# Performance work log

Hardware: AMD Instinct MI355X
Metric: run time of the kernel (lower is better)

Reference implementation:

```python
import jax, jax.numpy as jnp
import numpy as np

M = 8
EPS = 1e-5


def _bn(x, gamma, beta):
    # x: [T, N, C]; torch BatchNorm1d on [T, C, N] (training mode) normalizes
    # over batch and length dims -> axes (0, 1) here, biased variance.
    mean = jnp.mean(x, axis=(0, 1))
    var = jnp.var(x, axis=(0, 1))
    return (x - mean) * jax.lax.rsqrt(var + EPS) * gamma + beta


def setup_inputs() -> dict:
    key = jax.random.key(0)
    T, N, E = 128, 256, 128
    ks = jax.random.split(key, 16)
    s = 1.0 / np.sqrt(E)
    inp = {
        "node": jax.random.normal(ks[0], (T, N, E), dtype=jnp.float32),
        "Wq": jax.random.uniform(ks[1], (E, E), jnp.float32, -s, s),
        "bq": jax.random.uniform(ks[2], (E,), jnp.float32, -s, s),
        "Wk": jax.random.uniform(ks[3], (E, E), jnp.float32, -s, s),
        "bk": jax.random.uniform(ks[4], (E,), jnp.float32, -s, s),
        "Wv": jax.random.uniform(ks[5], (E, E), jnp.float32, -s, s),
        "bv": jax.random.uniform(ks[6], (E,), jnp.float32, -s, s),
        "Ww": jax.random.uniform(ks[7], (E, E), jnp.float32, -s, s),
        "bw": jax.random.uniform(ks[8], (E,), jnp.float32, -s, s),
        "Wf1": jax.random.uniform(ks[9], (4 * E, E), jnp.float32, -s, s),
        "bf1": jax.random.uniform(ks[10], (4 * E,), jnp.float32, -s, s),
        "Wf2": jax.random.uniform(ks[11], (E, 4 * E), jnp.float32, -0.5 * s, 0.5 * s),
        "bf2": jax.random.uniform(ks[12], (E,), jnp.float32, -0.5 * s, 0.5 * s),
        "g1": jnp.ones((E,), jnp.float32),
        "be1": jnp.zeros((E,), jnp.float32),
        "g2": jnp.ones((E,), jnp.float32),
        "be2": jnp.zeros((E,), jnp.float32),
        "temp_len": T,
    }
    return inp


def reference(node, Wq, bq, Wk, bk, Wv, bv, Ww, bw, Wf1, bf1, Wf2, bf2,
              g1, be1, g2, be2, temp_len):
    T, N, E = node.shape
    D = E // M          # head dim = 16
    dk = E / M          # softmax scale denominator (embedding_size / M)

    q = (node @ Wq.T + bq).reshape(T, N, M, D)
    k = (node @ Wk.T + bk).reshape(T, N, M, D)
    v = (node @ Wv.T + bv).reshape(T, N, M, D)

    # scores[t,n,j,m] = sum_d q[t,n,m,d]*k[t,j,m,d] / sqrt(dk)
    scores = jnp.einsum('tnmd,tjmd->tnjm', q, k) / jnp.sqrt(jnp.float32(dk))
    attn = jax.nn.softmax(scores, axis=2)  # softmax over key dim (dim=2)

    # out[t,n,m,d] = sum_j attn[t,n,j,m] * v[t,j,m,d]
    out = jnp.einsum('tnjm,tjmd->tnmd', attn, v).reshape(T, N, E)

    x = out @ Ww.T + bw + node
    x = _bn(x, g1, be1)

    x1 = jax.nn.relu(x @ Wf1.T + bf1) @ Wf2.T + bf2
    x = x + x1
    x = _bn(x, g2, be2)
    return x
```

## Files before the change

### kernel.cpp

```cpp
#include <hip/hip_runtime.h>
#include <stdint.h>

typedef unsigned int  uint32;
typedef unsigned short u16;
typedef __attribute__((ext_vector_type(8))) short short8;
typedef __attribute__((ext_vector_type(4))) float f32x4;
typedef __attribute__((ext_vector_type(4))) _Float16 half4;

__device__ __forceinline__ float bits2f(uint32 u){ union{uint32 u; float f;} c; c.u=u; return c.f; }
__device__ __forceinline__ uint32 f2bits(float f){ union{uint32 u; float f;} c; c.f=f; return c.u; }
__device__ __forceinline__ u16 f2b(float f){ uint32 u=f2bits(f); return (u16)((u + 0x7FFFu + ((u>>16)&1u))>>16); }
__device__ __forceinline__ float b2f(u16 h){ return bits2f(((uint32)h)<<16); }
__device__ __forceinline__ u16 f2h(float f){ _Float16 h=(_Float16)f; union{u16 u; _Float16 h;} c; c.h=h; return c.u; }
__device__ __forceinline__ float4 ld4f(const float* p){ return *(const float4*)p; }
#define BLO(u) bits2f((u)<<16)
#define BHI(u) bits2f((u)&0xFFFF0000u)

__global__ __launch_bounds__(256)
void cvt_w(const float4* __restrict__ wq, const float4* __restrict__ wk,
           const float4* __restrict__ wv, const float4* __restrict__ ww,
           const float4* __restrict__ wf1, const float4* __restrict__ wf2,
           u16* __restrict__ wb)
{
  const int i = blockIdx.x * 256 + threadIdx.x;
  const float4* src;
  if      (i <  4096) src = wq  + i;
  else if (i <  8192) src = wk  + (i-4096);
  else if (i < 12288) src = wv  + (i-8192);
  else if (i < 16384) src = ww  + (i-12288);
  else if (i < 32768) src = wf1 + (i-16384);
  else                src = wf2 + (i-32768);
  float4 v = *src;
  uint2 o;
  o.x = (uint32)f2b(v.x) | ((uint32)f2b(v.y) << 16);
  o.y = (uint32)f2b(v.z) | ((uint32)f2b(v.w) << 16);
  *(uint2*)(wb + (size_t)i*4) = o;
}

__device__ __forceinline__ void load_ab(const float* __restrict__ gacc,
                                        const float* __restrict__ gam,
                                        const float* __restrict__ bet,
                                        float* sA, float* sB, int t)
{
  if (t < 128) {
    const float mean = gacc[t] * (1.f/32768.f);
    const float var  = gacc[128 + t] * (1.f/32768.f) - mean * mean;
    const float rstd = rsqrtf(var + 1e-5f);
    const float Ac = gam[t] * rstd;
    sA[t] = Ac;
    sB[t] = bet[t] - mean * Ac;
  }
  __syncthreads();
}

template<int OMODE, int RES, bool RELU, bool AF32, bool BNA, bool STATS, bool ISQKV, int JT>
__global__ __launch_bounds__(256)
void gemm_k(const void* __restrict__ Ain,
            const u16* __restrict__ W0, const u16* __restrict__ W1, const u16* __restrict__ W2,
            const float* __restrict__ b0, const float* __restrict__ b1, const float* __restrict__ b2,
            const void* __restrict__ res,
            const float* __restrict__ gacc_in, const float* __restrict__ gam,
            const float* __restrict__ bet, float* __restrict__ gacc_out,
            void* __restrict__ O0, void* __restrict__ O1, void* __restrict__ O2,
            int K, int Nout, float qscale)
{
  constexpr int WROWS = JT * 32;
  __shared__ u16 As[128*72];
  __shared__ u16 Ws[WROWS*72];
  __shared__ __align__(16) float sA[128], sB[128];
  __shared__ float pS[128], pQ[128];
  const int t = threadIdx.x;
  const int row0 = blockIdx.x * 128;

  const u16* W = W0; const float* bias = b0; void* out = O0;
  float oscale = 1.f;
  int omode = OMODE, col0 = 0;
  if constexpr (ISQKV) {
    if (blockIdx.y == 1) { W = W1; bias = b1; out = O1; }
    if (blockIdx.y == 2) { W = W2; bias = b2; out = O2; omode = 3; }
    if (blockIdx.y == 0) oscale = qscale;
  } else {
    col0 = blockIdx.y * WROWS;
  }

  if constexpr (BNA || RES == 3) load_ab(gacc_in, gam, bet, sA, sB, t);

  const int L = t & 63, w = t >> 6;
  const int wrow = (w >> 1) * 64, wcol = (w & 1) * (JT * 16);
  const int lm = L & 15, lg = L >> 4;

  f32x4 acc[4][JT];
#pragma unroll
  for (int i = 0; i < 4; ++i)
#pragma unroll
    for (int j = 0; j < JT; ++j) acc[i][j] = (f32x4){0.f,0.f,0.f,0.f};

  const int srow = t >> 1, skc = (t & 1) * 32;
  const u16*   Ab = (const u16*)Ain + (size_t)(row0 + srow) * K + skc;
  const float* Af = (const float*)Ain + (size_t)(row0 + srow) * K + skc;
  u16* Asp = As + srow * 72 + skc;
  constexpr int TPR = 256 / WROWS;
  const int wsrow = t / TPR, wskc = (t % TPR) * (64 / TPR);
  const u16* Wp = W + (size_t)(col0 + wsrow) * K + wskc;
  u16* Wsp = Ws + wsrow * 72 + wskc;
  constexpr int NW = (64 / TPR) / 8;

  for (int k0 = 0; k0 < K; k0 += 64) {
    short8 ga[4], gw[NW];
    if constexpr (AF32) {
#pragma unroll
      for (int i = 0; i < 4; ++i) {
        const float4 fa = ld4f(Af + k0 + i*8);
        const float4 fb = ld4f(Af + k0 + i*8 + 4);
        short8 s;
        s[0]=(short)f2b(fa.x); s[1]=(short)f2b(fa.y); s[2]=(short)f2b(fa.z); s[3]=(short)f2b(fa.w);
        s[4]=(short)f2b(fb.x); s[5]=(short)f2b(fb.y); s[6]=(short)f2b(fb.z); s[7]=(short)f2b(fb.w);
        ga[i] = s;
      }
    } else if constexpr (BNA) {
#pragma unroll
      for (int i = 0; i < 4; ++i) {
        const int c = skc + k0 + i*8;
        const short8 x8 = *(const short8*)(Ab + k0 + i*8);
        const float4 A0 = *(const float4*)&sA[c], A1 = *(const float4*)&sA[c+4];
        const float4 B0 = *(const float4*)&sB[c], B1 = *(const float4*)&sB[c+4];
        short8 s;
        s[0]=(short)f2b(b2f((u16)x8[0])*A0.x+B0.x); s[1]=(short)f2b(b2f((u16)x8[1])*A0.y+B0.y);
        s[2]=(short)f2b(b2f((u16)x8[2])*A0.z+B0.z); s[3]=(short)f2b(b2f((u16)x8[3])*A0.w+B0.w);
        s[4]=(short)f2b(b2f((u16)x8[4])*A1.x+B1.x); s[5]=(short)f2b(b2f((u16)x8[5])*A1.y+B1.y);
        s[6]=(short)f2b(b2f((u16)x8[6])*A1.z+B1.z); s[7]=(short)f2b(b2f((u16)x8[7])*A1.w+B1.w);
        ga[i] = s;
      }
    } else {
#pragma unroll
      for (int i = 0; i < 4; ++i) ga[i] = *(const short8*)(Ab + k0 + i*8);
    }
#pragma unroll
    for (int i = 0; i < NW; ++i) gw[i] = *(const short8*)(Wp + k0 + i*8);
    __syncthreads();
#pragma unroll
    for (int i = 0; i < 4; ++i) *(short8*)(Asp + i*8) = ga[i];
#pragma unroll
    for (int i = 0; i < NW; ++i) *(short8*)(Wsp + i*8) = gw[i];
    __syncthreads();
#pragma unroll
    for (int ks = 0; ks < 64; ks += 32) {
      short8 af[4], wf[JT];
#pragma unroll
      for (int i = 0; i < 4; ++i)
        af[i] = *(const short8*)(As + (wrow + i*16 + lm) * 72 + ks + lg*8);
#pragma unroll
      for (int j = 0; j < JT; ++j)
        wf[j] = *(const short8*)(Ws + (wcol + j*16 + lm) * 72 + ks + lg*8);
#pragma unroll
      for (int i = 0; i < 4; ++i)
#pragma unroll
        for (int j = 0; j < JT; ++j)
          acc[i][j] = __builtin_amdgcn_mfma_f32_16x16x32_bf16(af[i], wf[j], acc[i][j], 0, 0, 0);
    }
  }

  float bj[JT];
#pragma unroll
  for (int j = 0; j < JT; ++j) bj[j] = bias[col0 + wcol + j*16 + lm];

  float stS[JT], stQ[JT];
#pragma unroll
  for (int j = 0; j < JT; ++j) { stS[j] = 0.f; stQ[j] = 0.f; }

#pragma unroll
  for (int i = 0; i < 4; ++i) {
    const int rowb = row0 + wrow + i*16 + lg*4;
#pragma unroll
    for (int j = 0; j < JT; ++j) {
      const int col = col0 + wcol + j*16 + lm;
      float ra = 0.f, rb = 0.f;
      if constexpr (RES == 3) { ra = sA[col & 127]; rb = sB[col & 127]; }
      if (omode == 3) {
        const int tt = rowb >> 8, n0 = rowb & 255;
        const int mh = col >> 4, d = col & 15;
        uint2 o;
        o.x = (uint32)f2h(acc[i][j][0] + bj[j]) | ((uint32)f2h(acc[i][j][1] + bj[j]) << 16);
        o.y = (uint32)f2h(acc[i][j][2] + bj[j]) | ((uint32)f2h(acc[i][j][3] + bj[j]) << 16);
        *(uint2*)((u16*)out + (((size_t)tt*8 + mh)*16 + d)*256 + n0) = o;
      } else {
#pragma unroll
        for (int r = 0; r < 4; ++r) {
          const int row = rowb + r;
          float v = acc[i][j][r] + bj[j];
          if constexpr (RES == 1) v += ((const float*)res)[(size_t)row*128 + col];
          if constexpr (RES == 3) v += b2f(((const u16*)res)[(size_t)row*128 + col]) * ra + rb;
          if constexpr (RELU) v = fmaxf(v, 0.f);
          if constexpr (STATS) { stS[j] += v; stQ[j] += v*v; }
          if (omode == 2) {
            const int tt = row >> 8, n = row & 255, mh = col >> 4, d = col & 15;
            ((u16*)out)[(((size_t)tt*8 + mh)*256 + n)*16 + d] = f2h(v * oscale);
          } else {
            ((u16*)out)[(size_t)row * Nout + col] = f2b(v);
          }
        }
      }
    }
  }

  if constexpr (STATS) {
    __syncthreads();
    if (t < 128) { pS[t] = 0.f; pQ[t] = 0.f; }
    __syncthreads();
#pragma unroll
    for (int j = 0; j < JT; ++j) {
      const int col = col0 + wcol + j*16 + lm;
      atomicAdd(&pS[col], stS[j]);
      atomicAdd(&pQ[col], stQ[j]);
    }
    __syncthreads();
    if (t < 128) {
      atomicAdd(&gacc_out[t],       pS[t]);
      atomicAdd(&gacc_out[128 + t], pQ[t]);
    }
  }
}

#define QKS 24
__global__ __launch_bounds__(256)
void attn_k(const u16* __restrict__ q, const u16* __restrict__ k,
            const u16* __restrict__ v, u16* __restrict__ ab)
{
  __shared__ __align__(16) u16 Qs[256*QKS];
  __shared__ __align__(16) u16 Ks[256*QKS];
  __shared__ __align__(16) u16 Vt[16*264];
  const int tm = blockIdx.x, tt = tm >> 3, m = tm & 7;
  const int t = threadIdx.x;

  const uint4* qg = (const uint4*)(q + (size_t)tm*4096);
  const uint4* kg = (const uint4*)(k + (size_t)tm*4096);
  const uint4* vg = (const uint4*)(v + (size_t)tm*4096);
#pragma unroll
  for (int p = t; p < 512; p += 256) {
    const uint4 a = qg[p], b = kg[p], c = vg[p];
    const int row = p >> 1, h = (p & 1) * 8;
    *(uint4*)(Qs + row*QKS + h) = a;
    *(uint4*)(Ks + row*QKS + h) = b;
    *(uint4*)(Vt + (p >> 5)*264 + (p & 31)*8) = c;
  }
  __syncthreads();

  const int w = t >> 6, L = t & 63, lm = L & 15, quad = L >> 4;

  half4 vf[16];
#pragma unroll
  for (int jt = 0; jt < 16; ++jt)
    vf[jt] = *(const half4*)(Vt + lm*264 + jt*16 + quad*4);

  for (int nt = 0; nt < 4; ++nt) {
    const half4 bq = *(const half4*)(Qs + ((w*4 + nt)*16 + lm)*QKS + quad*4);
    f32x4 s[16];
#pragma unroll
    for (int jt = 0; jt < 16; ++jt) {
      const half4 af = *(const half4*)(Ks + (jt*16 + lm)*QKS + quad*4);
      s[jt] = __builtin_amdgcn_mfma_f32_16x16x16f16(af, bq, (f32x4){0.f,0.f,0.f,0.f}, 0, 0, 0);
    }
    float mx = s[0][0];
#pragma unroll
    for (int jt = 0; jt < 16; ++jt)
#pragma unroll
      for (int r = 0; r < 4; ++r) mx = fmaxf(mx, s[jt][r]);
    mx = fmaxf(mx, __shfl_xor(mx, 16));
    mx = fmaxf(mx, __shfl_xor(mx, 32));
    float ls = 0.f;
#pragma unroll
    for (int jt = 0; jt < 16; ++jt)
#pragma unroll
      for (int r = 0; r < 4; ++r) { const float p = exp2f(s[jt][r] - mx); s[jt][r] = p; ls += p; }
    ls += __shfl_xor(ls, 16);
    ls += __shfl_xor(ls, 32);

    f32x4 oacc = {0.f,0.f,0.f,0.f};
#pragma unroll
    for (int jt = 0; jt < 16; ++jt) {
      half4 pf;
      pf[0] = (_Float16)s[jt][0]; pf[1] = (_Float16)s[jt][1];
      pf[2] = (_Float16)s[jt][2]; pf[3] = (_Float16)s[jt][3];
      oacc = __builtin_amdgcn_mfma_f32_16x16x16f16(pf, vf[jt], oacc, 0, 0, 0);
    }
    const int q0 = w*64 + nt*16 + quad*4;
#pragma unroll
    for (int r = 0; r < 4; ++r) {
      const float lr = __shfl(ls, quad*4 + r);
      ab[((size_t)tt*256 + q0 + r)*128 + m*16 + lm] = f2b(oacc[r] / lr);
    }
  }
}

__global__ __launch_bounds__(256)
void bn_final(const uint32* __restrict__ x2, const float* __restrict__ gacc,
              const float* __restrict__ gam, const float* __restrict__ bet,
              float* __restrict__ out)
{
  __shared__ float sA[128], sB[128];
  const int t = threadIdx.x;
  load_ab(gacc, gam, bet, sA, sB, t);
#pragma unroll 4
  for (int kk = 0; kk < 32; ++kk) {
    const size_t idx = (size_t)blockIdx.x * 8192 + kk * 256 + t;
    const uint32 u = x2[idx];
    const int c = (int)((idx & 63) * 2);
    float2 o;
    o.x = BLO(u) * sA[c]   + sB[c];
    o.y = BHI(u) * sA[c+1] + sB[c+1];
    ((float2*)out)[idx] = o;
  }
}

extern "C" void kernel_launch(void* const* d_in, const int* in_sizes, int n_in,
                              void* d_out, int out_size, void* d_ws, size_t ws_size,
                              hipStream_t stream)
{
  (void)in_sizes; (void)n_in; (void)out_size; (void)ws_size;
  const float* node = (const float*)d_in[0];
  const float* Wq  = (const float*)d_in[1];  const float* bq  = (const float*)d_in[2];
  const float* Wk  = (const float*)d_in[3];  const float* bk  = (const float*)d_in[4];
  const float* Wv  = (const float*)d_in[5];  const float* bv  = (const float*)d_in[6];
  const float* Ww  = (const float*)d_in[7];  const float* bw  = (const float*)d_in[8];
  const float* Wf1 = (const float*)d_in[9];  const float* bf1 = (const float*)d_in[10];
  const float* Wf2 = (const float*)d_in[11]; const float* bf2 = (const float*)d_in[12];
  const float* g1  = (const float*)d_in[13]; const float* be1 = (const float*)d_in[14];
  const float* g2  = (const float*)d_in[15]; const float* be2 = (const float*)d_in[16];
  float* out = (float*)d_out;
  char* ws = (char*)d_ws;

  u16* wb  = (u16*)(ws + 0);
  u16* qb  = (u16*)(ws + 524288);
  u16* kb  = (u16*)(ws + 8912896);
  u16* vb  = (u16*)(ws + 17301504);
  u16* ab  = (u16*)(ws + 25690112);
  u16* xb  = (u16*)(ws + 34078720);
  u16* x2b = (u16*)(ws + 42467328);
  float* accbuf = (float*)(ws + 50855936);
  u16* hb  = qb;

  u16* wqb = wb;          u16* wkb = wb + 16384;  u16* wvb = wb + 32768;
  u16* wwb = wb + 49152;  u16* wf1b = wb + 65536; u16* wf2b = wb + 131072;

  dim3 blk(256);
  const float QSCALE = 0.36067376022224085f;

  hipMemsetAsync(accbuf, 0, 512 * sizeof(float), stream);
  cvt_w<<<dim3(192), blk, 0, stream>>>((const float4*)Wq, (const float4*)Wk,
      (const float4*)Wv, (const float4*)Ww, (const float4*)Wf1, (const float4*)Wf2, wb);

  gemm_k<2,0,false,true,false,false,true,4><<<dim3(256,3), blk, 0, stream>>>(
      node, wqb,wkb,wvb, bq,bk,bv, nullptr, nullptr,nullptr,nullptr,nullptr,
      qb,kb,vb, 128, 128, QSCALE);

  attn_k<<<dim3(1024), blk, 0, stream>>>(qb, kb, vb, ab);

  gemm_k<0,1,false,false,false,true,false,4><<<dim3(256,1), blk, 0, stream>>>(
      ab, wwb,wwb,wwb, bw,bw,bw, node, nullptr,nullptr,nullptr, accbuf,
      xb,xb,xb, 128, 128, 1.f);

  gemm_k<0,0,true,false,true,false,false,4><<<dim3(256,4), blk, 0, stream>>>(
      xb, wf1b,wf1b,wf1b, bf1,bf1,bf1, nullptr, accbuf,g1,be1, nullptr,
      hb,hb,hb, 128, 512, 1.f);

  gemm_k<0,3,false,false,false,true,false,2><<<dim3(256,2), blk, 0, stream>>>(
      hb, wf2b,wf2b,wf2b, bf2,bf2,bf2, xb, accbuf,g1,be1, accbuf + 256,
      x2b,x2b,x2b, 512, 128, 1.f);

  bn_final<<<dim3(256), blk, 0, stream>>>((const uint32*)x2b, accbuf + 256, g2, be2, out);
}
```

Measured before the change: 209.0 us.

## Fuse all stages into one persistent kernel with software grid barriers

Merges the weight conversion, QKV GEMM, attention, output projection, FFN GEMMs and final batch-norm into one persistent kernel of 512 blocks. Stages are separated by an atomic-counter grid barrier and work is distributed with grid-stride loops over tiles. This removes six kernel launches and the gaps between them. In exchange it depends on all 512 blocks being co-resident (launch bounds set to 2 blocks per CU), adds spin-wait barrier cost, and uses a union of shared memory that may lower occupancy.

```diff
diff --git a/kernel.cpp b/kernel.cpp
--- a/kernel.cpp
+++ b/kernel.cpp
@@ -16,25 +16,58 @@
 #define BLO(u) bits2f((u)<<16)
 #define BHI(u) bits2f((u)&0xFFFF0000u)
 
-__global__ __launch_bounds__(256)
-void cvt_w(const float4* __restrict__ wq, const float4* __restrict__ wk,
-           const float4* __restrict__ wv, const float4* __restrict__ ww,
-           const float4* __restrict__ wf1, const float4* __restrict__ wf2,
-           u16* __restrict__ wb)
-{
-  const int i = blockIdx.x * 256 + threadIdx.x;
+#define QKS 24
+#define GRID 512
+
+struct Params {
+  const float* node;
+  const float *Wq,*bq,*Wk,*bk,*Wv,*bv,*Ww,*bw,*Wf1,*bf1,*Wf2,*bf2;
+  const float *g1,*be1,*g2,*be2;
+  float* out;
+  u16 *wb, *qb, *kb, *vb, *ab, *xb, *x2b, *hb;
+  float* accbuf;
+  int *cnt, *gen;
+};
+
+union SharedU {
+  struct { u16 As[128*72]; u16 Ws[128*72]; } g;
+  struct { u16 Qs[256*QKS]; u16 Ks[256*QKS]; u16 Vt[16*264]; } a;
+};
+
+__device__ __forceinline__ void gbar(int* cnt, int* gen)
+{
+  __syncthreads();
+  if (threadIdx.x == 0) {
+    __threadfence();
+    const int g = __hip_atomic_load(gen, __ATOMIC_RELAXED, __HIP_MEMORY_SCOPE_AGENT);
+    const int a = __hip_atomic_fetch_add(cnt, 1, __ATOMIC_ACQ_REL, __HIP_MEMORY_SCOPE_AGENT);
+    if (a == GRID - 1) {
+      __hip_atomic_store(cnt, 0, __ATOMIC_RELAXED, __HIP_MEMORY_SCOPE_AGENT);
+      __hip_atomic_fetch_add(gen, 1, __ATOMIC_RELEASE, __HIP_MEMORY_SCOPE_AGENT);
+    } else {
+      while (__hip_atomic_load(gen, __ATOMIC_RELAXED, __HIP_MEMORY_SCOPE_AGENT) == g)
+        __builtin_amdgcn_s_sleep(8);
+    }
+    __threadfence();
+  }
+  __syncthreads();
+}
+
+__device__ __forceinline__ void cvt_job(const Params& p, int j, int t)
+{
+  const int i = j * 256 + t;
   const float4* src;
-  if      (i <  4096) src = wq  + i;
-  else if (i <  8192) src = wk  + (i-4096);
-  else if (i < 12288) src = wv  + (i-8192);
-  else if (i < 16384) src = ww  + (i-12288);
-  else if (i < 32768) src = wf1 + (i-16384);
-  else                src = wf2 + (i-32768);
+  if      (i <  4096) src = (const float4*)p.Wq  + i;
+  else if (i <  8192) src = (const float4*)p.Wk  + (i-4096);
+  else if (i < 12288) src = (const float4*)p.Wv  + (i-8192);
+  else if (i < 16384) src = (const float4*)p.Ww  + (i-12288);
+  else if (i < 32768) src = (const float4*)p.Wf1 + (i-16384);
+  else                src = (const float4*)p.Wf2 + (i-32768);
   float4 v = *src;
   uint2 o;
   o.x = (uint32)f2b(v.x) | ((uint32)f2b(v.y) << 16);
   o.y = (uint32)f2b(v.z) | ((uint32)f2b(v.w) << 16);
-  *(uint2*)(wb + (size_t)i*4) = o;
+  *(uint2*)(p.wb + (size_t)i*4) = o;
 }
 
 __device__ __forceinline__ void load_ab(const float* __restrict__ gacc,
@@ -53,38 +86,16 @@
   __syncthreads();
 }
 
-template<int OMODE, int RES, bool RELU, bool AF32, bool BNA, bool STATS, bool ISQKV, int JT>
-__global__ __launch_bounds__(256)
-void gemm_k(const void* __restrict__ Ain,
-            const u16* __restrict__ W0, const u16* __restrict__ W1, const u16* __restrict__ W2,
-            const float* __restrict__ b0, const float* __restrict__ b1, const float* __restrict__ b2,
-            const void* __restrict__ res,
-            const float* __restrict__ gacc_in, const float* __restrict__ gam,
-            const float* __restrict__ bet, float* __restrict__ gacc_out,
-            void* __restrict__ O0, void* __restrict__ O1, void* __restrict__ O2,
-            int K, int Nout, float qscale)
+template<int OMODE, int RES, bool RELU, bool AF32, bool BNA, bool STATS, int JT>
+__device__ __forceinline__ void gemm_tile(
+    SharedU* Up, const float* sA, const float* sB, float* pS, float* pQ,
+    const void* Ain, const u16* W, const float* bias, const void* res,
+    float* gacc_out, void* out, int row0, int col0, int K, int Nout,
+    float oscale, int t)
 {
   constexpr int WROWS = JT * 32;
-  __shared__ u16 As[128*72];
-  __shared__ u16 Ws[WROWS*72];
-  __shared__ __align__(16) float sA[128], sB[128];
-  __shared__ float pS[128], pQ[128];
-  const int t = threadIdx.x;
-  const int row0 = blockIdx.x * 128;
-
-  const u16* W = W0; const float* bias = b0; void* out = O0;
-  float oscale = 1.f;
-  int omode = OMODE, col0 = 0;
-  if constexpr (ISQKV) {
-    if (blockIdx.y == 1) { W = W1; bias = b1; out = O1; }
-    if (blockIdx.y == 2) { W = W2; bias = b2; out = O2; omode = 3; }
-    if (blockIdx.y == 0) oscale = qscale;
-  } else {
-    col0 = blockIdx.y * WROWS;
-  }
-
-  if constexpr (BNA || RES == 3) load_ab(gacc_in, gam, bet, sA, sB, t);
-
+  u16* As = Up->g.As;
+  u16* Ws = Up->g.Ws;
   const int L = t & 63, w = t >> 6;
   const int wrow = (w >> 1) * 64, wcol = (w & 1) * (JT * 16);
   const int lm = L & 15, lg = L >> 4;
@@ -176,7 +187,7 @@
       const int col = col0 + wcol + j*16 + lm;
       float ra = 0.f, rb = 0.f;
       if constexpr (RES == 3) { ra = sA[col & 127]; rb = sB[col & 127]; }
-      if (omode == 3) {
+      if constexpr (OMODE == 3) {
         const int tt = rowb >> 8, n0 = rowb & 255;
         const int mh = col >> 4, d = col & 15;
         uint2 o;
@@ -192,7 +203,7 @@
           if constexpr (RES == 3) v += b2f(((const u16*)res)[(size_t)row*128 + col]) * ra + rb;
           if constexpr (RELU) v = fmaxf(v, 0.f);
           if constexpr (STATS) { stS[j] += v; stQ[j] += v*v; }
-          if (omode == 2) {
+          if constexpr (OMODE == 2) {
             const int tt = row >> 8, n = row & 255, mh = col >> 4, d = col & 15;
             ((u16*)out)[(((size_t)tt*8 + mh)*256 + n)*16 + d] = f2h(v * oscale);
           } else {
@@ -221,20 +232,16 @@
   }
 }
 
-#define QKS 24
-__global__ __launch_bounds__(256)
-void attn_k(const u16* __restrict__ q, const u16* __restrict__ k,
-            const u16* __restrict__ v, u16* __restrict__ ab)
-{
-  __shared__ __align__(16) u16 Qs[256*QKS];
-  __shared__ __align__(16) u16 Ks[256*QKS];
-  __shared__ __align__(16) u16 Vt[16*264];
-  const int tm = blockIdx.x, tt = tm >> 3, m = tm & 7;
-  const int t = threadIdx.x;
+__device__ __forceinline__ void attn_job(SharedU* Up, const u16* q, const u16* k,
+                                         const u16* v, u16* ab, int tm, int t)
+{
+  u16* Qs = Up->a.Qs; u16* Ks = Up->a.Ks; u16* Vt = Up->a.Vt;
+  const int tt = tm >> 3, m = tm & 7;
 
   const uint4* qg = (const uint4*)(q + (size_t)tm*4096);
   const uint4* kg = (const uint4*)(k + (size_t)tm*4096);
   const uint4* vg = (const uint4*)(v + (size_t)tm*4096);
+  __syncthreads();
 #pragma unroll
   for (int p = t; p < 512; p += 256) {
     const uint4 a = qg[p], b = kg[p], c = vg[p];
@@ -292,23 +299,69 @@
   }
 }
 
-__global__ __launch_bounds__(256)
-void bn_final(const uint32* __restrict__ x2, const float* __restrict__ gacc,
-              const float* __restrict__ gam, const float* __restrict__ bet,
-              float* __restrict__ out)
-{
-  __shared__ float sA[128], sB[128];
-  const int t = threadIdx.x;
-  load_ab(gacc, gam, bet, sA, sB, t);
+__global__ __launch_bounds__(256, 2)
+void fused_k(Params p)
+{
+  __shared__ __align__(16) SharedU U;
+  __shared__ __align__(16) float sA[128], sB[128];
+  __shared__ float pS[128], pQ[128];
+  const int t = threadIdx.x, bid = blockIdx.x;
+  const float QSCALE = 0.36067376022224085f;
+
+  const u16* wqb = p.wb;          const u16* wkb = p.wb + 16384;  const u16* wvb = p.wb + 32768;
+  const u16* wwb = p.wb + 49152;  const u16* wf1b = p.wb + 65536; const u16* wf2b = p.wb + 131072;
+
+  for (int j = bid; j < 192; j += GRID) cvt_job(p, j, t);
+  gbar(p.cnt, p.gen);
+
+  for (int j = bid; j < 768; j += GRID) {
+    const int x = j & 255, y = j >> 8;
+    if (y == 0)
+      gemm_tile<2,0,false,true,false,false,4>(&U,sA,sB,pS,pQ, p.node, wqb, p.bq,
+          nullptr, nullptr, p.qb, x*128, 0, 128, 128, QSCALE, t);
+    else if (y == 1)
+      gemm_tile<2,0,false,true,false,false,4>(&U,sA,sB,pS,pQ, p.node, wkb, p.bk,
+          nullptr, nullptr, p.kb, x*128, 0, 128, 128, 1.f, t);
+    else
+      gemm_tile<3,0,false,true,false,false,4>(&U,sA,sB,pS,pQ, p.node, wvb, p.bv,
+          nullptr, nullptr, p.vb, x*128, 0, 128, 128, 1.f, t);
+  }
+  gbar(p.cnt, p.gen);
+
+  for (int j = bid; j < 1024; j += GRID) attn_job(&U, p.qb, p.kb, p.vb, p.ab, j, t);
+  gbar(p.cnt, p.gen);
+
+  for (int j = bid; j < 256; j += GRID)
+    gemm_tile<0,1,false,false,false,true,4>(&U,sA,sB,pS,pQ, p.ab, wwb, p.bw,
+        p.node, p.accbuf, p.xb, j*128, 0, 128, 128, 1.f, t);
+  gbar(p.cnt, p.gen);
+
+  load_ab(p.accbuf, p.g1, p.be1, sA, sB, t);
+  for (int j = bid; j < 1024; j += GRID) {
+    const int x = j & 255, cy = j >> 8;
+    gemm_tile<0,0,true,false,true,false,4>(&U,sA,sB,pS,pQ, p.xb, wf1b, p.bf1,
+        nullptr, nullptr, p.hb, x*128, cy*128, 128, 512, 1.f, t);
+  }
+  gbar(p.cnt, p.gen);
+
+  for (int j = bid; j < 512; j += GRID)
+    gemm_tile<0,3,false,false,false,true,2>(&U,sA,sB,pS,pQ, p.hb, wf2b, p.bf2,
+        p.xb, p.accbuf + 256, p.x2b, (j >> 1)*128, (j & 1)*64, 512, 128, 1.f, t);
+  gbar(p.cnt, p.gen);
+
+  load_ab(p.accbuf + 256, p.g2, p.be2, sA, sB, t);
+  const uint32* x2 = (const uint32*)p.x2b;
+  for (int j = bid; j < 512; j += GRID) {
 #pragma unroll 4
-  for (int kk = 0; kk < 32; ++kk) {
-    const size_t idx = (size_t)blockIdx.x * 8192 + kk * 256 + t;
-    const uint32 u = x2[idx];
-    const int c = (int)((idx & 63) * 2);
-    float2 o;
-    o.x = BLO(u) * sA[c]   + sB[c];
-    o.y = BHI(u) * sA[c+1] + sB[c+1];
-    ((float2*)out)[idx] = o;
+    for (int kk = 0; kk < 16; ++kk) {
+      const size_t idx = (size_t)j * 4096 + kk * 256 + t;
+      const uint32 u = x2[idx];
+      const int c = (int)((idx & 63) * 2);
+      float2 o;
+      o.x = BLO(u) * sA[c]   + sB[c];
+      o.y = BHI(u) * sA[c+1] + sB[c+1];
+      ((float2*)p.out)[idx] = o;
+    }
   }
 }
 
@@ -317,55 +370,33 @@
                               hipStream_t stream)
 {
   (void)in_sizes; (void)n_in; (void)out_size; (void)ws_size;
-  const float* node = (const float*)d_in[0];
-  const float* Wq  = (const float*)d_in[1];  const float* bq  = (const float*)d_in[2];
-  const float* Wk  = (const float*)d_in[3];  const float* bk  = (const float*)d_in[4];
-  const float* Wv  = (const float*)d_in[5];  const float* bv  = (const float*)d_in[6];
-  const float* Ww  = (const float*)d_in[7];  const float* bw  = (const float*)d_in[8];
-  const float* Wf1 = (const float*)d_in[9];  const float* bf1 = (const float*)d_in[10];
-  const float* Wf2 = (const float*)d_in[11]; const float* bf2 = (const float*)d_in[12];
-  const float* g1  = (const float*)d_in[13]; const float* be1 = (const float*)d_in[14];
-  const float* g2  = (const float*)d_in[15]; const float* be2 = (const float*)d_in[16];
-  float* out = (float*)d_out;
   char* ws = (char*)d_ws;
 
-  u16* wb  = (u16*)(ws + 0);
-  u16* qb  = (u16*)(ws + 524288);
-  u16* kb  = (u16*)(ws + 8912896);
-  u16* vb  = (u16*)(ws + 17301504);
-  u16* ab  = (u16*)(ws + 25690112);
-  u16* xb  = (u16*)(ws + 34078720);
-  u16* x2b = (u16*)(ws + 42467328);
-  float* accbuf = (float*)(ws + 50855936);
-  u16* hb  = qb;
-
-  u16* wqb = wb;          u16* wkb = wb + 16384;  u16* wvb = wb + 32768;
-  u16* wwb = wb + 49152;  u16* wf1b = wb + 65536; u16* wf2b = wb + 131072;
-
-  dim3 blk(256);
-  const float QSCALE = 0.36067376022224085f;
-
-  hipMemsetAsync(accbuf, 0, 512 * sizeof(float), stream);
-  cvt_w<<<dim3(192), blk, 0, stream>>>((const float4*)Wq, (const float4*)Wk,
-      (const float4*)Wv, (const float4*)Ww, (const float4*)Wf1, (const float4*)Wf2, wb);
-
-  gemm_k<2,0,false,true,false,false,true,4><<<dim3(256,3), blk, 0, stream>>>(
-      node, wqb,wkb,wvb, bq,bk,bv, nullptr, nullptr,nullptr,nullptr,nullptr,
-      qb,kb,vb, 128, 128, QSCALE);
-
-  attn_k<<<dim3(1024), blk, 0, stream>>>(qb, kb, vb, ab);
-
-  gemm_k<0,1,false,false,false,true,false,4><<<dim3(256,1), blk, 0, stream>>>(
-      ab, wwb,wwb,wwb, bw,bw,bw, node, nullptr,nullptr,nullptr, accbuf,
-      xb,xb,xb, 128, 128, 1.f);
-
-  gemm_k<0,0,true,false,true,false,false,4><<<dim3(256,4), blk, 0, stream>>>(
-      xb, wf1b,wf1b,wf1b, bf1,bf1,bf1, nullptr, accbuf,g1,be1, nullptr,
-      hb,hb,hb, 128, 512, 1.f);
-
-  gemm_k<0,3,false,false,false,true,false,2><<<dim3(256,2), blk, 0, stream>>>(
-      hb, wf2b,wf2b,wf2b, bf2,bf2,bf2, xb, accbuf,g1,be1, accbuf + 256,
-      x2b,x2b,x2b, 512, 128, 1.f);
-
-  bn_final<<<dim3(256), blk, 0, stream>>>((const uint32*)x2b, accbuf + 256, g2, be2, out);
-}
+  Params P;
+  P.node = (const float*)d_in[0];
+  P.Wq  = (const float*)d_in[1];  P.bq  = (const float*)d_in[2];
+  P.Wk  = (const float*)d_in[3];  P.bk  = (const float*)d_in[4];
+  P.Wv  = (const float*)d_in[5];  P.bv  = (const float*)d_in[6];
+  P.Ww  = (const float*)d_in[7];  P.bw  = (const float*)d_in[8];
+  P.Wf1 = (const float*)d_in[9];  P.bf1 = (const float*)d_in[10];
+  P.Wf2 = (const float*)d_in[11]; P.bf2 = (const float*)d_in[12];
+  P.g1  = (const float*)d_in[13]; P.be1 = (const float*)d_in[14];
+  P.g2  = (const float*)d_in[15]; P.be2 = (const float*)d_in[16];
+  P.out = (float*)d_out;
+
+  P.wb  = (u16*)(ws + 0);
+  P.qb  = (u16*)(ws + 524288);
+  P.kb  = (u16*)(ws + 8912896);
+  P.vb  = (u16*)(ws + 17301504);
+  P.ab  = (u16*)(ws + 25690112);
+  P.xb  = (u16*)(ws + 34078720);
+  P.x2b = (u16*)(ws + 42467328);
+  P.accbuf = (float*)(ws + 50855936);
+  P.cnt = (int*)(ws + 50855936 + 2048);
+  P.gen = (int*)(ws + 50855936 + 2052);
+  P.hb  = P.qb;
+
+  hipMemsetAsync(ws + 50855936, 0, 4096, stream);
+
+  fused_k<<<dim3(GRID), dim3(256), 0, stream>>>(P);
+}
```

Result: slower. 579.5 us (+177.3%).

## Fuse weight conversion, memset and QKV GEMM into one launch

Applied to the files above, without the earlier changes.

Removes the separate memset and weight-conversion kernel. The QKV projection now reads fp32 weights and converts them inline, while extra blocks in the same launch convert the remaining weights to bf16 and zero the stats accumulators. GEMM kernels become per-stage wrappers around a shared device tile routine with compile-time output modes, and bn_final uses twice as many blocks. This cuts launch count and serial dependencies, at the cost of each QKV block re-converting the fp32 weights.

```diff
diff --git a/kernel.cpp b/kernel.cpp
--- a/kernel.cpp
+++ b/kernel.cpp
@@ -16,26 +16,7 @@
 #define BLO(u) bits2f((u)<<16)
 #define BHI(u) bits2f((u)&0xFFFF0000u)
 
-__global__ __launch_bounds__(256)
-void cvt_w(const float4* __restrict__ wq, const float4* __restrict__ wk,
-           const float4* __restrict__ wv, const float4* __restrict__ ww,
-           const float4* __restrict__ wf1, const float4* __restrict__ wf2,
-           u16* __restrict__ wb)
-{
-  const int i = blockIdx.x * 256 + threadIdx.x;
-  const float4* src;
-  if      (i <  4096) src = wq  + i;
-  else if (i <  8192) src = wk  + (i-4096);
-  else if (i < 12288) src = wv  + (i-8192);
-  else if (i < 16384) src = ww  + (i-12288);
-  else if (i < 32768) src = wf1 + (i-16384);
-  else                src = wf2 + (i-32768);
-  float4 v = *src;
-  uint2 o;
-  o.x = (uint32)f2b(v.x) | ((uint32)f2b(v.y) << 16);
-  o.y = (uint32)f2b(v.z) | ((uint32)f2b(v.w) << 16);
-  *(uint2*)(wb + (size_t)i*4) = o;
-}
+#define QKS 24
 
 __device__ __forceinline__ void load_ab(const float* __restrict__ gacc,
                                         const float* __restrict__ gam,
@@ -53,38 +34,14 @@
   __syncthreads();
 }
 
-template<int OMODE, int RES, bool RELU, bool AF32, bool BNA, bool STATS, bool ISQKV, int JT>
-__global__ __launch_bounds__(256)
-void gemm_k(const void* __restrict__ Ain,
-            const u16* __restrict__ W0, const u16* __restrict__ W1, const u16* __restrict__ W2,
-            const float* __restrict__ b0, const float* __restrict__ b1, const float* __restrict__ b2,
-            const void* __restrict__ res,
-            const float* __restrict__ gacc_in, const float* __restrict__ gam,
-            const float* __restrict__ bet, float* __restrict__ gacc_out,
-            void* __restrict__ O0, void* __restrict__ O1, void* __restrict__ O2,
-            int K, int Nout, float qscale)
+template<int OMODE, int RES, bool RELU, bool AF32, bool WF32, bool BNA, bool STATS, int JT>
+__device__ __forceinline__ void gemm_tile(
+    u16* As, u16* Ws, const float* sA, const float* sB, float* pS, float* pQ,
+    const void* Ain, const void* W, const float* bias, const void* res,
+    float* gacc_out, void* out, int row0, int col0, int K, int Nout,
+    float oscale, int t)
 {
   constexpr int WROWS = JT * 32;
-  __shared__ u16 As[128*72];
-  __shared__ u16 Ws[WROWS*72];
-  __shared__ __align__(16) float sA[128], sB[128];
-  __shared__ float pS[128], pQ[128];
-  const int t = threadIdx.x;
-  const int row0 = blockIdx.x * 128;
-
-  const u16* W = W0; const float* bias = b0; void* out = O0;
-  float oscale = 1.f;
-  int omode = OMODE, col0 = 0;
-  if constexpr (ISQKV) {
-    if (blockIdx.y == 1) { W = W1; bias = b1; out = O1; }
-    if (blockIdx.y == 2) { W = W2; bias = b2; out = O2; omode = 3; }
-    if (blockIdx.y == 0) oscale = qscale;
-  } else {
-    col0 = blockIdx.y * WROWS;
-  }
-
-  if constexpr (BNA || RES == 3) load_ab(gacc_in, gam, bet, sA, sB, t);
-
   const int L = t & 63, w = t >> 6;
   const int wrow = (w >> 1) * 64, wcol = (w & 1) * (JT * 16);
   const int lm = L & 15, lg = L >> 4;
@@ -101,7 +58,8 @@
   u16* Asp = As + srow * 72 + skc;
   constexpr int TPR = 256 / WROWS;
   const int wsrow = t / TPR, wskc = (t % TPR) * (64 / TPR);
-  const u16* Wp = W + (size_t)(col0 + wsrow) * K + wskc;
+  const u16*   Wp  = (const u16*)W + (size_t)(col0 + wsrow) * K + wskc;
+  const float* Wpf = (const float*)W + (size_t)(col0 + wsrow) * K + wskc;
   u16* Wsp = Ws + wsrow * 72 + wskc;
   constexpr int NW = (64 / TPR) / 8;
 
@@ -135,8 +93,20 @@
 #pragma unroll
       for (int i = 0; i < 4; ++i) ga[i] = *(const short8*)(Ab + k0 + i*8);
     }
-#pragma unroll
-    for (int i = 0; i < NW; ++i) gw[i] = *(const short8*)(Wp + k0 + i*8);
+    if constexpr (WF32) {
+#pragma unroll
+      for (int i = 0; i < NW; ++i) {
+        const float4 fa = ld4f(Wpf + k0 + i*8);
+        const float4 fb = ld4f(Wpf + k0 + i*8 + 4);
+        short8 s;
+        s[0]=(short)f2b(fa.x); s[1]=(short)f2b(fa.y); s[2]=(short)f2b(fa.z); s[3]=(short)f2b(fa.w);
+        s[4]=(short)f2b(fb.x); s[5]=(short)f2b(fb.y); s[6]=(short)f2b(fb.z); s[7]=(short)f2b(fb.w);
+        gw[i] = s;
+      }
+    } else {
+#pragma unroll
+      for (int i = 0; i < NW; ++i) gw[i] = *(const short8*)(Wp + k0 + i*8);
+    }
     __syncthreads();
 #pragma unroll
     for (int i = 0; i < 4; ++i) *(short8*)(Asp + i*8) = ga[i];
@@ -176,7 +146,7 @@
       const int col = col0 + wcol + j*16 + lm;
       float ra = 0.f, rb = 0.f;
       if constexpr (RES == 3) { ra = sA[col & 127]; rb = sB[col & 127]; }
-      if (omode == 3) {
+      if constexpr (OMODE == 3) {
         const int tt = rowb >> 8, n0 = rowb & 255;
         const int mh = col >> 4, d = col & 15;
         uint2 o;
@@ -192,7 +162,7 @@
           if constexpr (RES == 3) v += b2f(((const u16*)res)[(size_t)row*128 + col]) * ra + rb;
           if constexpr (RELU) v = fmaxf(v, 0.f);
           if constexpr (STATS) { stS[j] += v; stQ[j] += v*v; }
-          if (omode == 2) {
+          if constexpr (OMODE == 2) {
             const int tt = row >> 8, n = row & 255, mh = col >> 4, d = col & 15;
             ((u16*)out)[(((size_t)tt*8 + mh)*256 + n)*16 + d] = f2h(v * oscale);
           } else {
@@ -221,7 +191,94 @@
   }
 }
 
-#define QKS 24
+__global__ __launch_bounds__(256)
+void qkv_k(const float* __restrict__ node,
+           const float* __restrict__ Wq, const float* __restrict__ bq,
+           const float* __restrict__ Wk, const float* __restrict__ bk,
+           const float* __restrict__ Wv, const float* __restrict__ bv,
+           const float* __restrict__ Ww, const float* __restrict__ Wf1,
+           const float* __restrict__ Wf2,
+           u16* __restrict__ qb, u16* __restrict__ kb, u16* __restrict__ vb,
+           u16* __restrict__ wb, float* __restrict__ accbuf)
+{
+  const int bid = blockIdx.x, t = threadIdx.x;
+  if (bid < 768) {
+    __shared__ u16 As[128*72];
+    __shared__ u16 Ws[128*72];
+    __shared__ __align__(16) float sA[128], sB[128];
+    __shared__ float pS[128], pQ[128];
+    const int x = bid & 255, y = bid >> 8;
+    const float QSCALE = 0.36067376022224085f;
+    if (y == 0)
+      gemm_tile<2,0,false,true,true,false,false,4>(As,Ws,sA,sB,pS,pQ, node, Wq, bq,
+          nullptr, nullptr, qb, x*128, 0, 128, 128, QSCALE, t);
+    else if (y == 1)
+      gemm_tile<2,0,false,true,true,false,false,4>(As,Ws,sA,sB,pS,pQ, node, Wk, bk,
+          nullptr, nullptr, kb, x*128, 0, 128, 128, 1.f, t);
+    else
+      gemm_tile<3,0,false,true,true,false,false,4>(As,Ws,sA,sB,pS,pQ, node, Wv, bv,
+          nullptr, nullptr, vb, x*128, 0, 128, 128, 1.f, t);
+  } else if (bid < 912) {
+    const int i = (bid - 768) * 256 + t;
+    const float4* src; u16* dst;
+    if      (i <  4096) { src = (const float4*)Ww  + i;         dst = wb +  49152 + (size_t)i*4; }
+    else if (i < 20480) { src = (const float4*)Wf1 + (i-4096);  dst = wb +  65536 + (size_t)(i-4096)*4; }
+    else                { src = (const float4*)Wf2 + (i-20480); dst = wb + 131072 + (size_t)(i-20480)*4; }
+    float4 v = *src;
+    uint2 o;
+    o.x = (uint32)f2b(v.x) | ((uint32)f2b(v.y) << 16);
+    o.y = (uint32)f2b(v.z) | ((uint32)f2b(v.w) << 16);
+    *(uint2*)dst = o;
+  } else {
+    accbuf[t] = 0.f;
+    accbuf[256 + t] = 0.f;
+  }
+}
+
+__global__ __launch_bounds__(256)
+void oproj_k(const u16* __restrict__ ab, const u16* __restrict__ wwb,
+             const float* __restrict__ bw, const float* __restrict__ node,
+             float* __restrict__ accbuf, u16* __restrict__ xb)
+{
+  __shared__ u16 As[128*72];
+  __shared__ u16 Ws[128*72];
+  __shared__ __align__(16) float sA[128], sB[128];
+  __shared__ float pS[128], pQ[128];
+  gemm_tile<0,1,false,false,false,false,true,4>(As,Ws,sA,sB,pS,pQ, ab, wwb, bw,
+      node, accbuf, xb, blockIdx.x*128, 0, 128, 128, 1.f, threadIdx.x);
+}
+
+__global__ __launch_bounds__(256)
+void ffn1_k(const u16* __restrict__ xb, const u16* __restrict__ wf1b,
+            const float* __restrict__ bf1, const float* __restrict__ accbuf,
+            const float* __restrict__ g1, const float* __restrict__ be1,
+            u16* __restrict__ hb)
+{
+  __shared__ u16 As[128*72];
+  __shared__ u16 Ws[128*72];
+  __shared__ __align__(16) float sA[128], sB[128];
+  __shared__ float pS[128], pQ[128];
+  load_ab(accbuf, g1, be1, sA, sB, threadIdx.x);
+  gemm_tile<0,0,true,false,false,true,false,4>(As,Ws,sA,sB,pS,pQ, xb, wf1b, bf1,
+      nullptr, nullptr, hb, blockIdx.x*128, blockIdx.y*128, 128, 512, 1.f, threadIdx.x);
+}
+
+__global__ __launch_bounds__(256)
+void ffn2_k(const u16* __restrict__ hb, const u16* __restrict__ wf2b,
+            const float* __restrict__ bf2, const u16* __restrict__ xb,
+            const float* __restrict__ accbuf, const float* __restrict__ g1,
+            const float* __restrict__ be1, float* __restrict__ acc2,
+            u16* __restrict__ x2b)
+{
+  __shared__ u16 As[128*72];
+  __shared__ u16 Ws[64*72];
+  __shared__ __align__(16) float sA[128], sB[128];
+  __shared__ float pS[128], pQ[128];
+  load_ab(accbuf, g1, be1, sA, sB, threadIdx.x);
+  gemm_tile<0,3,false,false,false,false,true,2>(As,Ws,sA,sB,pS,pQ, hb, wf2b, bf2,
+      xb, acc2, x2b, blockIdx.x*128, blockIdx.y*64, 512, 128, 1.f, threadIdx.x);
+}
+
 __global__ __launch_bounds__(256)
 void attn_k(const u16* __restrict__ q, const u16* __restrict__ k,
             const u16* __restrict__ v, u16* __restrict__ ab)
@@ -301,8 +358,8 @@
   const int t = threadIdx.x;
   load_ab(gacc, gam, bet, sA, sB, t);
 #pragma unroll 4
-  for (int kk = 0; kk < 32; ++kk) {
-    const size_t idx = (size_t)blockIdx.x * 8192 + kk * 256 + t;
+  for (int kk = 0; kk < 16; ++kk) {
+    const size_t idx = (size_t)blockIdx.x * 4096 + kk * 256 + t;
     const uint32 u = x2[idx];
     const int c = (int)((idx & 63) * 2);
     float2 o;
@@ -339,33 +396,16 @@
   float* accbuf = (float*)(ws + 50855936);
   u16* hb  = qb;
 
-  u16* wqb = wb;          u16* wkb = wb + 16384;  u16* wvb = wb + 32768;
   u16* wwb = wb + 49152;  u16* wf1b = wb + 65536; u16* wf2b = wb + 131072;
 
   dim3 blk(256);
-  const float QSCALE = 0.36067376022224085f;
-
-  hipMemsetAsync(accbuf, 0, 512 * sizeof(float), stream);
-  cvt_w<<<dim3(192), blk, 0, stream>>>((const float4*)Wq, (const float4*)Wk,
-      (const float4*)Wv, (const float4*)Ww, (const float4*)Wf1, (const float4*)Wf2, wb);
-
-  gemm_k<2,0,false,true,false,false,true,4><<<dim3(256,3), blk, 0, stream>>>(
-      node, wqb,wkb,wvb, bq,bk,bv, nullptr, nullptr,nullptr,nullptr,nullptr,
-      qb,kb,vb, 128, 128, QSCALE);
-
+
+  qkv_k<<<dim3(913), blk, 0, stream>>>(node, Wq,bq, Wk,bk, Wv,bv, Ww, Wf1, Wf2,
+                                       qb, kb, vb, wb, accbuf);
   attn_k<<<dim3(1024), blk, 0, stream>>>(qb, kb, vb, ab);
-
-  gemm_k<0,1,false,false,false,true,false,4><<<dim3(256,1), blk, 0, stream>>>(
-      ab, wwb,wwb,wwb, bw,bw,bw, node, nullptr,nullptr,nullptr, accbuf,
-      xb,xb,xb, 128, 128, 1.f);
-
-  gemm_k<0,0,true,false,true,false,false,4><<<dim3(256,4), blk, 0, stream>>>(
-      xb, wf1b,wf1b,wf1b, bf1,bf1,bf1, nullptr, accbuf,g1,be1, nullptr,
-      hb,hb,hb, 128, 512, 1.f);
-
-  gemm_k<0,3,false,false,false,true,false,2><<<dim3(256,2), blk, 0, stream>>>(
-      hb, wf2b,wf2b,wf2b, bf2,bf2,bf2, xb, accbuf,g1,be1, accbuf + 256,
-      x2b,x2b,x2b, 512, 128, 1.f);
-
-  bn_final<<<dim3(256), blk, 0, stream>>>((const uint32*)x2b, accbuf + 256, g2, be2, out);
-}
+  oproj_k<<<dim3(256), blk, 0, stream>>>(ab, wwb, bw, node, accbuf, xb);
+  ffn1_k<<<dim3(256,4), blk, 0, stream>>>(xb, wf1b, bf1, accbuf, g1, be1, hb);
+  ffn2_k<<<dim3(256,2), blk, 0, stream>>>(hb, wf2b, bf2, xb, accbuf, g1, be1,
+                                          accbuf + 256, x2b);
+  bn_final<<<dim3(512), blk, 0, stream>>>((const uint32*)x2b, accbuf + 256, g2, be2, out);
+}
```

After: 205.7 us. About the same (-1.6%).
